# Kernel tuning notes

Measured on AMD Instinct MI355X. Metric: run time of the kernel, lower is better.

The kernel has to match this reference:

```python
import jax, jax.numpy as jnp
import numpy as np

SQRT2 = 1.4142135623730951  # ScaleCostWeight(sqrt(2)) applied to residuals
N_ITERS = 10
DAMP = 1e-8  # tiny Tikhonov for numerical safety of the 6x6 solve


def _hat(phi):
    x, y, z = phi[0], phi[1], phi[2]
    o = jnp.zeros((), phi.dtype)
    return jnp.stack([jnp.stack([o, -z, y]),
                      jnp.stack([z, o, -x]),
                      jnp.stack([-y, x, o])])


def se3_exp(xi):
    # xi: [6] = [rho (trans), phi (rot)] -> 4x4 SE3 matrix
    rho, phi = xi[:3], xi[3:]
    theta2 = jnp.sum(phi * phi)
    small = theta2 < 1e-12
    theta2s = jnp.where(small, 1.0, theta2)  # double-where for safe grads
    theta = jnp.sqrt(theta2s)
    A = jnp.where(small, 1.0, jnp.sin(theta) / theta)
    B = jnp.where(small, 0.5, (1.0 - jnp.cos(theta)) / theta2s)
    C = jnp.where(small, 1.0 / 6.0, (theta - jnp.sin(theta)) / (theta2s * theta))
    K = _hat(phi)
    K2 = K @ K
    I3 = jnp.eye(3, dtype=xi.dtype)
    R = I3 + A * K + B * K2
    V = I3 + B * K + C * K2
    t = V @ rho
    top = jnp.concatenate([R, t[:, None]], axis=1)
    bot = jnp.array([[0.0, 0.0, 0.0, 1.0]], dtype=xi.dtype)
    return jnp.concatenate([top, bot], axis=0)


def se3_inv(T):
    R = T[..., :3, :3]
    t = T[..., :3, 3:]
    Rt = jnp.swapaxes(R, -1, -2)
    top = jnp.concatenate([Rt, -(Rt @ t)], axis=-1)
    bot = jnp.broadcast_to(jnp.array([0.0, 0.0, 0.0, 1.0], T.dtype),
                           T.shape[:-2] + (1, 4))
    return jnp.concatenate([top, bot], axis=-2)


def _r_single(xi, T, src3, trg3, Wh, w):
    # residual of one batch element at local perturbation xi (retract on right)
    Tn = T @ se3_exp(xi)
    pred = Tn[:3, :3] @ src3 + Tn[:3, 3:4]          # [3, N]
    e = trg3 - pred                                  # [3, N]
    ew = jnp.einsum('nij,jn->in', Wh, e) * w         # cholesky-weighted, w: [1,N]
    return (ew * SQRT2).reshape(-1)                  # [3N]


def _forward(src4, trg4, w, T_init, inv_cov, T_s_v):
    src3 = src4[:, :3, :]
    trg3 = trg4[:, :3, :]
    # W_half = cholesky(inv_cov)^T, computed once (aux var, constant over iters)
    Wh = jnp.swapaxes(jnp.linalg.cholesky(inv_cov), -1, -2)  # [B, N, 3, 3]
    B = src4.shape[0]
    I6 = jnp.eye(6, dtype=src4.dtype)

    def step(T, _):
        xi0 = jnp.zeros((B, 6), T.dtype)
        J = jax.vmap(jax.jacfwd(_r_single), in_axes=(0, 0, 0, 0, 0, 0))(
            xi0, T, src3, trg3, Wh, w)               # [B, 3N, 6]
        r = jax.vmap(_r_single)(xi0, T, src3, trg3, Wh, w)  # [B, 3N]
        g = jnp.einsum('bri,br->bi', J, r)
        H = jnp.einsum('bri,brj->bij', J, J) + DAMP * I6
        dx = -jnp.linalg.solve(H, g[..., None])[..., 0]
        return T @ jax.vmap(se3_exp)(dx), None

    T, _ = jax.lax.scan(step, T_init, None, length=N_ITERS)
    T_sv = jnp.broadcast_to(T_s_v, (B, 4, 4))
    return se3_inv(T_sv) @ T @ T_sv


def setup_inputs() -> dict:
    key = jax.random.key(0)
    B, N = 256, 2048
    k1, k2, k3, k4, k5, k6 = jax.random.split(key, 6)
    src3 = 2.0 * jax.random.normal(k1, (B, 3, N), dtype=jnp.float32)
    # well-posed registration problem: trg = T_true * src + noise
    T_true = jax.vmap(se3_exp)(0.3 * jax.random.normal(k2, (B, 6), dtype=jnp.float32))
    trg3 = (jnp.einsum('bij,bjn->bin', T_true[:, :3, :3], src3)
            + T_true[:, :3, 3:4]
            + 0.01 * jax.random.normal(k3, (B, 3, N), dtype=jnp.float32))
    ones = jnp.ones((B, 1, N), dtype=jnp.float32)
    keypoints_3D_src = jnp.concatenate([src3, ones], axis=1)
    keypoints_3D_trg = jnp.concatenate([trg3, ones], axis=1)
    weights = jax.random.uniform(k4, (B, 1, N), dtype=jnp.float32,
                                 minval=0.1, maxval=1.0)
    A = 0.3 * jax.random.normal(k5, (B, N, 3, 3), dtype=jnp.float32)
    inv_cov_weights = A @ jnp.swapaxes(A, -1, -2) + jnp.eye(3, dtype=jnp.float32)
    T_trg_src_init = jax.vmap(se3_exp)(
        0.05 * jax.random.normal(k6, (B, 6), dtype=jnp.float32))
    T_s_v = se3_exp(jnp.array([0.1, -0.2, 0.3, 0.2, -0.1, 0.15], dtype=jnp.float32))
    return {"keypoints_3D_src": keypoints_3D_src,
            "keypoints_3D_trg": keypoints_3D_trg,
            "weights": weights,
            "T_trg_src_init": T_trg_src_init,
            "inv_cov_weights": inv_cov_weights,
            "T_s_v": T_s_v}


def reference(keypoints_3D_src, keypoints_3D_trg, weights, T_trg_src_init,
              inv_cov_weights, T_s_v):
    return _forward(keypoints_3D_src, keypoints_3D_trg, weights,
                    T_trg_src_init, inv_cov_weights, T_s_v)
```

## Files before the change

kernel.cpp:

```cpp
#include <hip/hip_runtime.h>
#include <math.h>

#define NPTS   2048
#define BD1    256
#define SPLIT  2
#define PPB    (NPTS / SPLIT)
#define PPT    (PPB / BD1)
#define NMOM   72
#define NITERS 10
#define DAMPF  1e-8f

__launch_bounds__(BD1, 1)
__global__ void moments_kernel(const float* __restrict__ src4,
                               const float* __restrict__ trg4,
                               const float* __restrict__ wts,
                               const float* __restrict__ icov,
                               float* __restrict__ mom, int B)
{
    const int b   = blockIdx.x >> 1;
    const int s   = blockIdx.x & 1;
    const int tid = threadIdx.x;

    const float* srcb = src4 + (size_t)b * 4 * NPTS;
    const float* trgb = trg4 + (size_t)b * 4 * NPTS;
    const float* wb   = wts  + (size_t)b * NPTS;
    const float* cb   = icov + (size_t)b * NPTS * 9;

    float acc[NMOM];
    #pragma unroll
    for (int k = 0; k < NMOM; ++k) acc[k] = 0.0f;

    #pragma unroll 2
    for (int kk = 0; kk < PPT; ++kk) {
        int n = s * PPB + kk * BD1 + tid;
        float sx = srcb[n], sy = srcb[NPTS + n], sz = srcb[2 * NPTS + n];
        float gx = trgb[n], gy = trgb[NPTS + n], gz = trgb[2 * NPTS + n];
        float w  = wb[n];
        const float* c = cb + (size_t)n * 9;
        float w2 = 2.0f * w * w;
        float W[6];
        W[0] = w2 * c[0];
        W[1] = w2 * c[3];
        W[2] = w2 * c[6];
        W[3] = w2 * c[4];
        W[4] = w2 * c[7];
        W[5] = w2 * c[8];

        float hx = W[0] * gx + W[1] * gy + W[2] * gz;
        float hy = W[1] * gx + W[3] * gy + W[4] * gz;
        float hz = W[2] * gx + W[4] * gy + W[5] * gz;

        float sv[3] = { sx, sy, sz };
        float hv[3] = { hx, hy, hz };
        float ss[6] = { sx*sx, sx*sy, sx*sz, sy*sy, sy*sz, sz*sz };

        #pragma unroll
        for (int ij = 0; ij < 6; ++ij) {
            acc[ij] += W[ij];
            #pragma unroll
            for (int c2 = 0; c2 < 3; ++c2) acc[6 + ij * 3 + c2] += W[ij] * sv[c2];
            #pragma unroll
            for (int cd = 0; cd < 6; ++cd) acc[24 + ij * 6 + cd] += W[ij] * ss[cd];
        }
        acc[60] += hx; acc[61] += hy; acc[62] += hz;
        #pragma unroll
        for (int c2 = 0; c2 < 3; ++c2)
            #pragma unroll
            for (int i = 0; i < 3; ++i) acc[63 + c2 * 3 + i] += sv[c2] * hv[i];
    }

    __shared__ float lds[36][BD1 + 1];
    #pragma unroll
    for (int h = 0; h < 2; ++h) {
        if (h) __syncthreads();
        #pragma unroll
        for (int k = 0; k < 36; ++k) lds[k][tid] = acc[h * 36 + k];
        __syncthreads();
        if (tid < 36) {
            const float* row = lds[tid];
            float s0 = 0.f, s1 = 0.f, s2 = 0.f, s3 = 0.f;
            #pragma unroll 8
            for (int j = 0; j < BD1; j += 4) {
                s0 += row[j]; s1 += row[j + 1]; s2 += row[j + 2]; s3 += row[j + 3];
            }
            mom[((size_t)s * NMOM + h * 36 + tid) * B + b] = (s0 + s1) + (s2 + s3);
        }
    }
}

__launch_bounds__(64, 1)
__global__ void solve_kernel(const float* __restrict__ mom,
                             const float* __restrict__ Tinit,
                             const float* __restrict__ Tsv,
                             float* __restrict__ out, int B)
{
    const int b = blockIdx.x * 64 + threadIdx.x;
    if (b >= B) return;

    float m[NMOM];
    #pragma unroll
    for (int k = 0; k < NMOM; ++k)
        m[k] = mom[k * B + b] + mom[(NMOM + k) * B + b];

    float Rm[3][3], tv[3];
    #pragma unroll
    for (int i = 0; i < 3; ++i) {
        #pragma unroll
        for (int j = 0; j < 3; ++j) Rm[i][j] = Tinit[b * 16 + i * 4 + j];
        tv[i] = Tinit[b * 16 + i * 4 + 3];
    }

    const int SY[3][3] = { {0,1,2}, {1,3,4}, {2,4,5} };

    for (int it = 0; it < NITERS; ++it) {
        float C1[6][3];
        #pragma unroll
        for (int ij = 0; ij < 6; ++ij) {
            float a0 = m[6 + ij * 3 + 0], a1 = m[6 + ij * 3 + 1], a2 = m[6 + ij * 3 + 2];
            #pragma unroll
            for (int a = 0; a < 3; ++a)
                C1[ij][a] = Rm[a][0] * a0 + Rm[a][1] * a1 + Rm[a][2] * a2;
        }
        float SM[3][3], SWp[3];
        #pragma unroll
        for (int i = 0; i < 3; ++i) {
            SM[i][0] = C1[SY[i][1]][2] - C1[SY[i][2]][1];
            SM[i][1] = C1[SY[i][2]][0] - C1[SY[i][0]][2];
            SM[i][2] = C1[SY[i][0]][1] - C1[SY[i][1]][0];
            SWp[i]   = C1[SY[i][0]][0] + C1[SY[i][1]][1] + C1[SY[i][2]][2];
        }
        float P2[6][6];
        #pragma unroll
        for (int ij = 0; ij < 6; ++ij) {
            float S00 = m[24 + ij * 6 + 0], S01 = m[24 + ij * 6 + 1], S02 = m[24 + ij * 6 + 2];
            float S11 = m[24 + ij * 6 + 3], S12 = m[24 + ij * 6 + 4], S22 = m[24 + ij * 6 + 5];
            float U[3][3];
            #pragma unroll
            for (int a = 0; a < 3; ++a) {
                U[a][0] = Rm[a][0] * S00 + Rm[a][1] * S01 + Rm[a][2] * S02;
                U[a][1] = Rm[a][0] * S01 + Rm[a][1] * S11 + Rm[a][2] * S12;
                U[a][2] = Rm[a][0] * S02 + Rm[a][1] * S12 + Rm[a][2] * S22;
            }
            P2[0][ij] = U[0][0]*Rm[0][0] + U[0][1]*Rm[0][1] + U[0][2]*Rm[0][2];
            P2[1][ij] = U[0][0]*Rm[1][0] + U[0][1]*Rm[1][1] + U[0][2]*Rm[1][2];
            P2[2][ij] = U[0][0]*Rm[2][0] + U[0][1]*Rm[2][1] + U[0][2]*Rm[2][2];
            P2[3][ij] = U[1][0]*Rm[1][0] + U[1][1]*Rm[1][1] + U[1][2]*Rm[1][2];
            P2[4][ij] = U[1][0]*Rm[2][0] + U[1][1]*Rm[2][1] + U[1][2]*Rm[2][2];
            P2[5][ij] = U[2][0]*Rm[2][0] + U[2][1]*Rm[2][1] + U[2][2]*Rm[2][2];
        }
        float SN00 = -P2[5][3] + 2.f * P2[4][4] - P2[3][5];
        float SN01 = -P2[2][4] + P2[5][1] + P2[1][5] - P2[4][2];
        float SN02 = -P2[4][1] + P2[2][3] + P2[3][2] - P2[1][4];
        float SN11 =  2.f * P2[2][2] - P2[5][0] - P2[0][5];
        float SN12 =  P2[4][0] - P2[2][1] - P2[1][2] + P2[0][4];
        float SN22 = -P2[3][0] + 2.f * P2[1][1] - P2[0][3];

        float SWt0 = m[0]*tv[0] + m[1]*tv[1] + m[2]*tv[2];
        float SWt1 = m[1]*tv[0] + m[3]*tv[1] + m[4]*tv[2];
        float SWt2 = m[2]*tv[0] + m[4]*tv[1] + m[5]*tv[2];
        float Su[3] = { m[60] - SWp[0] - SWt0,
                        m[61] - SWp[1] - SWt1,
                        m[62] - SWp[2] - SWt2 };

        float G[3][3];
        #pragma unroll
        for (int a = 0; a < 3; ++a)
            #pragma unroll
            for (int bb = 0; bb < 3; ++bb)
                G[a][bb] = Rm[a][0]*m[63 + 0 + bb] + Rm[a][1]*m[63 + 3 + bb] + Rm[a][2]*m[63 + 6 + bb];
        float ch[3] = { G[1][2] - G[2][1], G[2][0] - G[0][2], G[0][1] - G[1][0] };
        float pw[3];
        pw[0] = P2[1][2] + P2[3][4] + P2[4][5] - P2[2][1] - P2[4][3] - P2[5][4];
        pw[1] = P2[2][0] + P2[4][1] + P2[5][2] - P2[0][2] - P2[1][4] - P2[2][5];
        pw[2] = P2[0][1] + P2[1][3] + P2[2][4] - P2[1][0] - P2[3][1] - P2[4][2];
        float Sq[3];
        #pragma unroll
        for (int i = 0; i < 3; ++i)
            Sq[i] = ch[i] - pw[i] + SM[0][i]*tv[0] + SM[1][i]*tv[1] + SM[2][i]*tv[2];

        float Hm[6][6];
        Hm[0][0] = m[0]; Hm[0][1] = m[1]; Hm[0][2] = m[2];
        Hm[1][1] = m[3]; Hm[1][2] = m[4]; Hm[2][2] = m[5];
        #pragma unroll
        for (int i = 0; i < 3; ++i) {
            Hm[i][3] = -SM[i][0]; Hm[i][4] = -SM[i][1]; Hm[i][5] = -SM[i][2];
        }
        Hm[3][3] = -SN00; Hm[3][4] = -SN01; Hm[3][5] = -SN02;
        Hm[4][4] = -SN11; Hm[4][5] = -SN12; Hm[5][5] = -SN22;
        #pragma unroll
        for (int i = 0; i < 6; ++i) {
            Hm[i][i] += DAMPF;
            #pragma unroll
            for (int j = 0; j < 6; ++j)
                if (j < i) Hm[i][j] = Hm[j][i];
        }
        float rhs[6] = { Su[0], Su[1], Su[2], Sq[0], Sq[1], Sq[2] };

        float L[6][6];
        #pragma unroll
        for (int i = 0; i < 6; ++i) {
            #pragma unroll
            for (int j = 0; j < 6; ++j) {
                if (j > i) continue;
                float sum = Hm[i][j];
                #pragma unroll
                for (int k2 = 0; k2 < 6; ++k2)
                    if (k2 < j) sum -= L[i][k2] * L[j][k2];
                if (i == j) L[i][i] = sqrtf(sum);
                else        L[i][j] = sum / L[j][j];
            }
        }
        float z[6];
        #pragma unroll
        for (int i = 0; i < 6; ++i) {
            float sum = rhs[i];
            #pragma unroll
            for (int k2 = 0; k2 < 6; ++k2)
                if (k2 < i) sum -= L[i][k2] * z[k2];
            z[i] = sum / L[i][i];
        }
        float y[6];
        #pragma unroll
        for (int i = 5; i >= 0; --i) {
            float sum = z[i];
            #pragma unroll
            for (int k2 = 0; k2 < 6; ++k2)
                if (k2 > i) sum -= L[k2][i] * y[k2];
            y[i] = sum / L[i][i];
        }

        float drx = Rm[0][0]*y[0] + Rm[1][0]*y[1] + Rm[2][0]*y[2];
        float dry = Rm[0][1]*y[0] + Rm[1][1]*y[1] + Rm[2][1]*y[2];
        float drz = Rm[0][2]*y[0] + Rm[1][2]*y[1] + Rm[2][2]*y[2];
        float dpx = Rm[0][0]*y[3] + Rm[1][0]*y[4] + Rm[2][0]*y[5];
        float dpy = Rm[0][1]*y[3] + Rm[1][1]*y[4] + Rm[2][1]*y[5];
        float dpz = Rm[0][2]*y[3] + Rm[1][2]*y[4] + Rm[2][2]*y[5];

        float th2  = dpx*dpx + dpy*dpy + dpz*dpz;
        bool  sm   = th2 < 1e-12f;
        float th2s = sm ? 1.0f : th2;
        float th   = sqrtf(th2s);
        float sth  = sinf(th), cth = cosf(th);
        float Ae = sm ? 1.0f : sth / th;
        float Be = sm ? 0.5f : (1.0f - cth) / th2s;
        float Ce = sm ? (1.0f / 6.0f) : (th - sth) / (th2s * th);
        float Rd00 = 1.0f + Be * (dpx*dpx - th2);
        float Rd01 = -Ae * dpz + Be * dpx * dpy;
        float Rd02 =  Ae * dpy + Be * dpx * dpz;
        float Rd10 =  Ae * dpz + Be * dpx * dpy;
        float Rd11 = 1.0f + Be * (dpy*dpy - th2);
        float Rd12 = -Ae * dpx + Be * dpy * dpz;
        float Rd20 = -Ae * dpy + Be * dpx * dpz;
        float Rd21 =  Ae * dpx + Be * dpy * dpz;
        float Rd22 = 1.0f + Be * (dpz*dpz - th2);
        float V00 = 1.0f + Ce * (dpx*dpx - th2);
        float V01 = -Be * dpz + Ce * dpx * dpy;
        float V02 =  Be * dpy + Ce * dpx * dpz;
        float V10 =  Be * dpz + Ce * dpx * dpy;
        float V11 = 1.0f + Ce * (dpy*dpy - th2);
        float V12 = -Be * dpx + Ce * dpy * dpz;
        float V20 = -Be * dpy + Ce * dpx * dpz;
        float V21 =  Be * dpx + Ce * dpy * dpz;
        float V22 = 1.0f + Ce * (dpz*dpz - th2);
        float tdx = V00 * drx + V01 * dry + V02 * drz;
        float tdy = V10 * drx + V11 * dry + V12 * drz;
        float tdz = V20 * drx + V21 * dry + V22 * drz;

        float nR[3][3];
        nR[0][0] = Rm[0][0]*Rd00 + Rm[0][1]*Rd10 + Rm[0][2]*Rd20;
        nR[0][1] = Rm[0][0]*Rd01 + Rm[0][1]*Rd11 + Rm[0][2]*Rd21;
        nR[0][2] = Rm[0][0]*Rd02 + Rm[0][1]*Rd12 + Rm[0][2]*Rd22;
        nR[1][0] = Rm[1][0]*Rd00 + Rm[1][1]*Rd10 + Rm[1][2]*Rd20;
        nR[1][1] = Rm[1][0]*Rd01 + Rm[1][1]*Rd11 + Rm[1][2]*Rd21;
        nR[1][2] = Rm[1][0]*Rd02 + Rm[1][1]*Rd12 + Rm[1][2]*Rd22;
        nR[2][0] = Rm[2][0]*Rd00 + Rm[2][1]*Rd10 + Rm[2][2]*Rd20;
        nR[2][1] = Rm[2][0]*Rd01 + Rm[2][1]*Rd11 + Rm[2][2]*Rd21;
        nR[2][2] = Rm[2][0]*Rd02 + Rm[2][1]*Rd12 + Rm[2][2]*Rd22;
        float ntx = Rm[0][0]*tdx + Rm[0][1]*tdy + Rm[0][2]*tdz + tv[0];
        float nty = Rm[1][0]*tdx + Rm[1][1]*tdy + Rm[1][2]*tdz + tv[1];
        float ntz = Rm[2][0]*tdx + Rm[2][1]*tdy + Rm[2][2]*tdz + tv[2];
        #pragma unroll
        for (int i = 0; i < 3; ++i)
            #pragma unroll
            for (int j = 0; j < 3; ++j) Rm[i][j] = nR[i][j];
        tv[0] = ntx; tv[1] = nty; tv[2] = ntz;
    }

    {
        float R00 = Rm[0][0], R01 = Rm[0][1], R02 = Rm[0][2];
        float R10 = Rm[1][0], R11 = Rm[1][1], R12 = Rm[1][2];
        float R20 = Rm[2][0], R21 = Rm[2][1], R22 = Rm[2][2];
        float tx = tv[0], ty = tv[1], tz = tv[2];

        float Rv00 = Tsv[0], Rv01 = Tsv[1], Rv02 = Tsv[2],  tvx = Tsv[3];
        float Rv10 = Tsv[4], Rv11 = Tsv[5], Rv12 = Tsv[6],  tvy = Tsv[7];
        float Rv20 = Tsv[8], Rv21 = Tsv[9], Rv22 = Tsv[10], tvz = Tsv[11];

        float P00 = R00*Rv00 + R01*Rv10 + R02*Rv20;
        float P01 = R00*Rv01 + R01*Rv11 + R02*Rv21;
        float P02 = R00*Rv02 + R01*Rv12 + R02*Rv22;
        float P10 = R10*Rv00 + R11*Rv10 + R12*Rv20;
        float P11 = R10*Rv01 + R11*Rv11 + R12*Rv21;
        float P12 = R10*Rv02 + R11*Rv12 + R12*Rv22;
        float P20 = R20*Rv00 + R21*Rv10 + R22*Rv20;
        float P21 = R20*Rv01 + R21*Rv11 + R22*Rv21;
        float P22 = R20*Rv02 + R21*Rv12 + R22*Rv22;
        float Ptx = R00*tvx + R01*tvy + R02*tvz + tx;
        float Pty = R10*tvx + R11*tvy + R12*tvz + ty;
        float Ptz = R20*tvx + R21*tvy + R22*tvz + tz;

        float ex = Ptx - tvx, ey = Pty - tvy, ez = Ptz - tvz;
        float* o = out + (size_t)b * 16;
        o[0]  = Rv00*P00 + Rv10*P10 + Rv20*P20;
        o[1]  = Rv00*P01 + Rv10*P11 + Rv20*P21;
        o[2]  = Rv00*P02 + Rv10*P12 + Rv20*P22;
        o[3]  = Rv00*ex  + Rv10*ey  + Rv20*ez;
        o[4]  = Rv01*P00 + Rv11*P10 + Rv21*P20;
        o[5]  = Rv01*P01 + Rv11*P11 + Rv21*P21;
        o[6]  = Rv01*P02 + Rv11*P12 + Rv21*P22;
        o[7]  = Rv01*ex  + Rv11*ey  + Rv21*ez;
        o[8]  = Rv02*P00 + Rv12*P10 + Rv22*P20;
        o[9]  = Rv02*P01 + Rv12*P11 + Rv22*P21;
        o[10] = Rv02*P02 + Rv12*P12 + Rv22*P22;
        o[11] = Rv02*ex  + Rv12*ey  + Rv22*ez;
        o[12] = 0.0f; o[13] = 0.0f; o[14] = 0.0f; o[15] = 1.0f;
    }
}

extern "C" void kernel_launch(void* const* d_in, const int* in_sizes, int n_in,
                              void* d_out, int out_size, void* d_ws, size_t ws_size,
                              hipStream_t stream)
{
    const float* src4  = (const float*)d_in[0];
    const float* trg4  = (const float*)d_in[1];
    const float* wts   = (const float*)d_in[2];
    const float* Tinit = (const float*)d_in[3];
    const float* icov  = (const float*)d_in[4];
    const float* Tsv   = (const float*)d_in[5];

    const int B = in_sizes[3] / 16;
    float* mom = (float*)d_ws;

    hipLaunchKernelGGL(moments_kernel, dim3(B * SPLIT), dim3(BD1), 0, stream,
                       src4, trg4, wts, icov, mom, B);
    hipLaunchKernelGGL(solve_kernel, dim3((B + 63) / 64), dim3(64), 0, stream,
                       mom, Tinit, Tsv, (float*)d_out, B);
}
```

Before: 110.1 us.

## Split moments across four blocks, raise occupancy, use fast math in solve

Each batch element's points are now split across four blocks instead of two, and the moments kernel's launch bounds allow three blocks per CU with the point loop fully unrolled. The solve kernel sums the four partial moment sets. In the solve it swaps sqrt and divides for hardware rsq and rcp and uses fast sin and cos, to shorten the serial per-thread chain. Costs are more partial-moment traffic, possible register pressure under the tighter bounds, and small precision loss from the approximate intrinsics.

```diff
diff --git a/kernel.cpp b/kernel.cpp
--- a/kernel.cpp
+++ b/kernel.cpp
@@ -3,22 +3,25 @@
 
 #define NPTS   2048
 #define BD1    256
-#define SPLIT  2
+#define SPLIT  4
 #define PPB    (NPTS / SPLIT)
 #define PPT    (PPB / BD1)
 #define NMOM   72
 #define NITERS 10
 #define DAMPF  1e-8f
 
-__launch_bounds__(BD1, 1)
+__device__ __forceinline__ float frcp(float x) { return __builtin_amdgcn_rcpf(x); }
+__device__ __forceinline__ float frsq(float x) { return __builtin_amdgcn_rsqf(x); }
+
+__launch_bounds__(BD1, 3)
 __global__ void moments_kernel(const float* __restrict__ src4,
                                const float* __restrict__ trg4,
                                const float* __restrict__ wts,
                                const float* __restrict__ icov,
                                float* __restrict__ mom, int B)
 {
-    const int b   = blockIdx.x >> 1;
-    const int s   = blockIdx.x & 1;
+    const int b   = blockIdx.x / SPLIT;
+    const int s   = blockIdx.x % SPLIT;
     const int tid = threadIdx.x;
 
     const float* srcb = src4 + (size_t)b * 4 * NPTS;
@@ -30,21 +33,23 @@
     #pragma unroll
     for (int k = 0; k < NMOM; ++k) acc[k] = 0.0f;
 
-    #pragma unroll 2
+    #pragma unroll
     for (int kk = 0; kk < PPT; ++kk) {
         int n = s * PPB + kk * BD1 + tid;
         float sx = srcb[n], sy = srcb[NPTS + n], sz = srcb[2 * NPTS + n];
         float gx = trgb[n], gy = trgb[NPTS + n], gz = trgb[2 * NPTS + n];
         float w  = wb[n];
         const float* c = cb + (size_t)n * 9;
+        float c0 = c[0], c3 = c[3], c4 = c[4], c6 = c[6], c7 = c[7], c8 = c[8];
+
         float w2 = 2.0f * w * w;
         float W[6];
-        W[0] = w2 * c[0];
-        W[1] = w2 * c[3];
-        W[2] = w2 * c[6];
-        W[3] = w2 * c[4];
-        W[4] = w2 * c[7];
-        W[5] = w2 * c[8];
+        W[0] = w2 * c0;
+        W[1] = w2 * c3;
+        W[2] = w2 * c6;
+        W[3] = w2 * c4;
+        W[4] = w2 * c7;
+        W[5] = w2 * c8;
 
         float hx = W[0] * gx + W[1] * gy + W[2] * gz;
         float hy = W[1] * gx + W[3] * gy + W[4] * gz;
@@ -99,8 +104,13 @@
 
     float m[NMOM];
     #pragma unroll
-    for (int k = 0; k < NMOM; ++k)
-        m[k] = mom[k * B + b] + mom[(NMOM + k) * B + b];
+    for (int k = 0; k < NMOM; ++k) {
+        float v = 0.0f;
+        #pragma unroll
+        for (int s = 0; s < SPLIT; ++s)
+            v += mom[((size_t)s * NMOM + k) * B + b];
+        m[k] = v;
+    }
 
     float Rm[3][3], tv[3];
     #pragma unroll
@@ -197,6 +207,7 @@
         float rhs[6] = { Su[0], Su[1], Su[2], Sq[0], Sq[1], Sq[2] };
 
         float L[6][6];
+        float invD[6];
         #pragma unroll
         for (int i = 0; i < 6; ++i) {
             #pragma unroll
@@ -206,8 +217,8 @@
                 #pragma unroll
                 for (int k2 = 0; k2 < 6; ++k2)
                     if (k2 < j) sum -= L[i][k2] * L[j][k2];
-                if (i == j) L[i][i] = sqrtf(sum);
-                else        L[i][j] = sum / L[j][j];
+                if (i == j) { invD[i] = frsq(sum); L[i][i] = sum * invD[i]; }
+                else        L[i][j] = sum * invD[j];
             }
         }
         float z[6];
@@ -217,7 +228,7 @@
             #pragma unroll
             for (int k2 = 0; k2 < 6; ++k2)
                 if (k2 < i) sum -= L[i][k2] * z[k2];
-            z[i] = sum / L[i][i];
+            z[i] = sum * invD[i];
         }
         float y[6];
         #pragma unroll
@@ -226,7 +237,7 @@
             #pragma unroll
             for (int k2 = 0; k2 < 6; ++k2)
                 if (k2 > i) sum -= L[k2][i] * y[k2];
-            y[i] = sum / L[i][i];
+            y[i] = sum * invD[i];
         }
 
         float drx = Rm[0][0]*y[0] + Rm[1][0]*y[1] + Rm[2][0]*y[2];
@@ -240,10 +251,12 @@
         bool  sm   = th2 < 1e-12f;
         float th2s = sm ? 1.0f : th2;
         float th   = sqrtf(th2s);
-        float sth  = sinf(th), cth = cosf(th);
-        float Ae = sm ? 1.0f : sth / th;
-        float Be = sm ? 0.5f : (1.0f - cth) / th2s;
-        float Ce = sm ? (1.0f / 6.0f) : (th - sth) / (th2s * th);
+        float ith  = frcp(th);
+        float ith2 = ith * ith;
+        float sth  = __sinf(th), cth = __cosf(th);
+        float Ae = sm ? 1.0f : sth * ith;
+        float Be = sm ? 0.5f : (1.0f - cth) * ith2;
+        float Ce = sm ? (1.0f / 6.0f) : (th - sth) * ith2 * ith;
         float Rd00 = 1.0f + Be * (dpx*dpx - th2);
         float Rd01 = -Ae * dpz + Be * dpx * dpy;
         float Rd02 =  Ae * dpy + Be * dpx * dpz;
```

Result: slower. 117.4 us (+6.6%).
